# Optimization experiments

Hardware: AMD Instinct MI355X
Metric: run time of the kernel (lower is better)

## Reference

```python
import jax, jax.numpy as jnp
import numpy as np

N, B, D, K_IN, P = 64, 256, 1792, 35, 10
EPS = 1e-5


def setup_inputs() -> dict:
    key = jax.random.key(0)
    ks = jax.random.split(key, 8)
    s_tok = 1.0 / np.sqrt(K_IN)
    s_net = 1.0 / np.sqrt(D)
    return {
        "X": jax.random.normal(ks[0], (N, B, D), dtype=jnp.float32),
        "task_id": jax.random.normal(ks[1], (B, K_IN), dtype=jnp.float32),
        # tokens: Linear(35, 10*1792)
        "W_tok": jax.random.uniform(ks[2], (P * D, K_IN), jnp.float32, -s_tok, s_tok),
        "b_tok": jax.random.uniform(ks[3], (P * D,), jnp.float32, -s_tok, s_tok),
        # ptokens: Linear(35, 1792)
        "W_ptok": jax.random.uniform(ks[4], (D, K_IN), jnp.float32, -s_tok, s_tok),
        "b_ptok": jax.random.uniform(ks[5], (D,), jnp.float32, -s_tok, s_tok),
        # LayerNorm(1792)
        "gamma": jnp.ones((D,), jnp.float32),
        "beta": jnp.zeros((D,), jnp.float32),
        # net: Linear(1792, 10)
        "W_net": jax.random.uniform(ks[6], (P, D), jnp.float32, -s_net, s_net),
        "b_net": jax.random.uniform(ks[7], (P,), jnp.float32, -s_net, s_net),
    }


def _layernorm(x, gamma, beta):
    mu = jnp.mean(x, axis=-1, keepdims=True)
    var = jnp.mean(jnp.square(x - mu), axis=-1, keepdims=True)
    return (x - mu) * jax.lax.rsqrt(var + EPS) * gamma + beta


def reference(X, task_id, W_tok, b_tok, W_ptok, b_ptok, gamma, beta, W_net, b_net):
    # ptokens(task_id): (b, D); identical across n, so compute once and broadcast.
    ptok = task_id @ W_ptok.T + b_ptok                       # (b, D)
    task_token = _layernorm(ptok[None, :, :] + X, gamma, beta)  # (n, b, D)
    # net -> sigmoid: per-token mixing weights over P prompts.
    weight = jax.nn.sigmoid(task_token @ W_net.T + b_net)    # (n, b, P)
    # tokens(task_id): (b, P, D); identical across n, broadcast in einsum.
    prompt_bank = (task_id @ W_tok.T + b_tok).reshape(B, P, D)  # (b, P, D)
    prompt = jnp.einsum("nbp,bpd->nbd", weight, prompt_bank)  # (n, b, D)
    return X + prompt
```

## Files before the change

kernel.cpp:

```cpp
#include <hip/hip_runtime.h>
#include <hip/hip_bf16.h>

#define NN 64
#define BB 256
#define DD 1792
#define KK 35
#define PP 10
#define DQ 448
#define MROWS 16
#define NCHUNK 4
#define NGRP 28

__device__ __forceinline__ float group16_sum_dpp(float x) {
    asm("v_add_f32_dpp %0, %0, %0 row_shr:1 row_mask:0xf bank_mask:0xf bound_ctrl:0" : "+v"(x));
    asm("v_add_f32_dpp %0, %0, %0 row_shr:2 row_mask:0xf bank_mask:0xf bound_ctrl:0" : "+v"(x));
    asm("v_add_f32_dpp %0, %0, %0 row_shr:4 row_mask:0xf bank_mask:0xf bound_ctrl:0" : "+v"(x));
    asm("v_add_f32_dpp %0, %0, %0 row_shr:8 row_mask:0xf bank_mask:0xf bound_ctrl:0" : "+v"(x));
    return x;
}

__global__ void prep_gf(const float* __restrict__ gamma, const float* __restrict__ beta,
                        const float* __restrict__ Wnet, const float* __restrict__ bnet,
                        float* __restrict__ GF, float* __restrict__ SG, float* __restrict__ ZC) {
    const int p = blockIdx.x;
    const int tid = threadIdx.x;
    float sg = 0.f, sb = 0.f;
#pragma unroll
    for (int j = 0; j < 7; ++j) {
        int d = j * 256 + tid;
        float wv = Wnet[p * DD + d];
        float g = gamma[d] * wv;
        GF[p * DD + d] = g;
        sg += g;
        sb += beta[d] * wv;
    }
#pragma unroll
    for (int off = 32; off > 0; off >>= 1) {
        sg += __shfl_xor(sg, off);
        sb += __shfl_xor(sb, off);
    }
    __shared__ float rs[4][2];
    if ((tid & 63) == 0) { rs[tid >> 6][0] = sg; rs[tid >> 6][1] = sb; }
    __syncthreads();
    if (tid == 0) {
        float a = 0.f, c = 0.f;
#pragma unroll
        for (int w = 0; w < 4; ++w) { a += rs[w][0]; c += rs[w][1]; }
        SG[p] = a;
        ZC[p] = c + bnet[p];
    }
}

__global__ void prep_bank(const float* __restrict__ task,
                          const float* __restrict__ Wtok, const float* __restrict__ btok,
                          const float* __restrict__ Wptok, const float* __restrict__ bptok,
                          float* __restrict__ bank, float* __restrict__ ptok) {
    __shared__ float ti[32 * KK];
    const int tid = threadIdx.x;
    const int b0 = blockIdx.y * 32;
    for (int i = tid; i < 32 * KK; i += 256) ti[i] = task[b0 * KK + i];

    const int r = blockIdx.x * 256 + tid;
    const bool isbank = (r < PP * DD);
    const int rr = isbank ? r : (r - PP * DD);
    const float* __restrict__ W = isbank ? Wtok : Wptok;
    const float bias = isbank ? btok[r] : bptok[rr];

    float w[KK];
#pragma unroll
    for (int k = 0; k < KK; ++k) w[k] = W[rr * KK + k];

    __syncthreads();
#pragma unroll 1
    for (int bb = 0; bb < 32; ++bb) {
        float acc = bias;
#pragma unroll
        for (int k = 0; k < KK; ++k) acc = fmaf(ti[bb * KK + k], w[k], acc);
        const int b = b0 + bb;
        if (isbank) bank[b * (PP * DD) + r] = acc;
        else        ptok[b * DD + rr]       = acc;
    }
}

__global__ __launch_bounds__(448) void main_kernel(
    const float* __restrict__ X, const float* __restrict__ BANK,
    const float* __restrict__ PTOK, const float* __restrict__ GF,
    const float* __restrict__ SG, const float* __restrict__ ZC,
    float* __restrict__ OUT) {
    const int tid = threadIdx.x;
    const int b = blockIdx.y;
    const int n0 = blockIdx.x * MROWS;

    const float4* __restrict__ X4 = (const float4*)X;
    const float4* __restrict__ B4 = (const float4*)BANK;
    const float4* __restrict__ G4 = (const float4*)GF;
    const float4* __restrict__ P4 = (const float4*)PTOK;
    float4* __restrict__ O4 = (float4*)OUT;

    __shared__ float red[MROWS][NGRP][12];
    __shared__ float wlds[MROWS][PP];

    float4 gf[PP];
#pragma unroll
    for (int p = 0; p < PP; ++p) gf[p] = G4[p * DQ + tid];
    const float4 ptk = P4[b * DQ + tid];

    const bool writer = ((tid & 15) == 15);
    const int g = tid >> 4;

    float4 xn = X4[((n0 + 0) * BB + b) * DQ + tid];
#pragma unroll 1
    for (int r = 0; r < MROWS; ++r) {
        float4 x = xn;
        if (r < MROWS - 1) xn = X4[((n0 + r + 1) * BB + b) * DQ + tid];

        float4 t;
        t.x = x.x + ptk.x; t.y = x.y + ptk.y; t.z = x.z + ptk.z; t.w = x.w + ptk.w;

        float s1 = t.x + t.y + t.z + t.w;
        float s2 = t.x * t.x;
        s2 = fmaf(t.y, t.y, s2); s2 = fmaf(t.z, t.z, s2); s2 = fmaf(t.w, t.w, s2);
        float a[PP];
#pragma unroll
        for (int p = 0; p < PP; ++p) {
            float v = t.x * gf[p].x;
            v = fmaf(t.y, gf[p].y, v);
            v = fmaf(t.z, gf[p].z, v);
            v = fmaf(t.w, gf[p].w, v);
            a[p] = v;
        }
        s1 = group16_sum_dpp(s1);
        s2 = group16_sum_dpp(s2);
#pragma unroll
        for (int p = 0; p < PP; ++p) a[p] = group16_sum_dpp(a[p]);

        if (writer) {
            float4* dst = (float4*)&red[r][g][0];
            dst[0] = make_float4(s1, s2, a[0], a[1]);
            dst[1] = make_float4(a[2], a[3], a[4], a[5]);
            dst[2] = make_float4(a[6], a[7], a[8], a[9]);
        }
    }
    __syncthreads();

    if (tid < 256) {
        const int row = tid >> 4;
        const int v = tid & 15;
        float f = 0.f;
        if (v < 12) {
#pragma unroll
            for (int q = 0; q < NGRP; ++q) f += red[row][q][v];
        }
        const int base = (tid & 63) & ~15;
        const float mu = __shfl(f, base)     * (1.0f / (float)DD);
        const float ms = __shfl(f, base + 1) * (1.0f / (float)DD);
        const float istd = rsqrtf(ms - mu * mu + 1e-5f);
        if (v >= 2 && v < 12) {
            const int p = v - 2;
            const float z = istd * (f - mu * SG[p]) + ZC[p];
            wlds[row][p] = 1.0f / (1.0f + __expf(-z));
        }
    }
    __syncthreads();

    float4 bk[PP];
#pragma unroll
    for (int p = 0; p < PP; ++p) bk[p] = B4[(b * PP + p) * DQ + tid];

#pragma unroll 4
    for (int r = MROWS - 1; r >= 0; --r) {
        const int idx = ((n0 + r) * BB + b) * DQ + tid;
        float4 acc = X4[idx];
#pragma unroll
        for (int p = 0; p < PP; ++p) {
            const float wv2 = wlds[r][p];
            acc.x = fmaf(wv2, bk[p].x, acc.x);
            acc.y = fmaf(wv2, bk[p].y, acc.y);
            acc.z = fmaf(wv2, bk[p].z, acc.z);
            acc.w = fmaf(wv2, bk[p].w, acc.w);
        }
        O4[idx] = acc;
    }
}

extern "C" void kernel_launch(void* const* d_in, const int* in_sizes, int n_in,
                              void* d_out, int out_size, void* d_ws, size_t ws_size,
                              hipStream_t stream) {
    const float* X     = (const float*)d_in[0];
    const float* task  = (const float*)d_in[1];
    const float* Wtok  = (const float*)d_in[2];
    const float* btok  = (const float*)d_in[3];
    const float* Wptok = (const float*)d_in[4];
    const float* bptok = (const float*)d_in[5];
    const float* gamma = (const float*)d_in[6];
    const float* beta  = (const float*)d_in[7];
    const float* Wnet  = (const float*)d_in[8];
    const float* bnet  = (const float*)d_in[9];
    float* out = (float*)d_out;

    float* ws = (float*)d_ws;
    float* bank = ws;
    float* ptok = ws + (size_t)BB * PP * DD;
    float* GF   = ptok + (size_t)BB * DD;
    float* SG   = GF + PP * DD;
    float* ZC   = SG + PP;

    prep_gf<<<PP, 256, 0, stream>>>(gamma, beta, Wnet, bnet, GF, SG, ZC);
    prep_bank<<<dim3(77, 8), 256, 0, stream>>>(task, Wtok, btok, Wptok, bptok, bank, ptok);
    main_kernel<<<dim3(NCHUNK, BB), 448, 0, stream>>>(X, bank, ptok, GF, SG, ZC, out);
}
```

Baseline: 91.93 us.

## Keep X rows in registers across two half-passes to avoid rereading X

The main kernel now processes its 16 rows in two halves of 8. Each half loads its 8 X rows into registers once, computes the LayerNorm and net reductions from them, then reuses the same registers for the output mix. Before, X was read a second time from global memory in the output phase. This raises register pressure (8 float4 rows plus 10 bank/gf float4), may lower occupancy, adds an extra pair of barriers per half, and reloads GF and the bank slice twice per block.

```diff
diff --git a/kernel.cpp b/kernel.cpp
--- a/kernel.cpp
+++ b/kernel.cpp
@@ -8,6 +8,7 @@
 #define PP 10
 #define DQ 448
 #define MROWS 16
+#define HROWS 8
 #define NCHUNK 4
 #define NGRP 28
 
@@ -97,89 +98,93 @@
     const float4* __restrict__ P4 = (const float4*)PTOK;
     float4* __restrict__ O4 = (float4*)OUT;
 
-    __shared__ float red[MROWS][NGRP][12];
-    __shared__ float wlds[MROWS][PP];
-
-    float4 gf[PP];
-#pragma unroll
-    for (int p = 0; p < PP; ++p) gf[p] = G4[p * DQ + tid];
+    __shared__ float red[HROWS][NGRP][12];
+    __shared__ float wlds[HROWS][PP];
+
     const float4 ptk = P4[b * DQ + tid];
-
     const bool writer = ((tid & 15) == 15);
     const int g = tid >> 4;
 
-    float4 xn = X4[((n0 + 0) * BB + b) * DQ + tid];
 #pragma unroll 1
-    for (int r = 0; r < MROWS; ++r) {
-        float4 x = xn;
-        if (r < MROWS - 1) xn = X4[((n0 + r + 1) * BB + b) * DQ + tid];
-
-        float4 t;
-        t.x = x.x + ptk.x; t.y = x.y + ptk.y; t.z = x.z + ptk.z; t.w = x.w + ptk.w;
-
-        float s1 = t.x + t.y + t.z + t.w;
-        float s2 = t.x * t.x;
-        s2 = fmaf(t.y, t.y, s2); s2 = fmaf(t.z, t.z, s2); s2 = fmaf(t.w, t.w, s2);
-        float a[PP];
-#pragma unroll
-        for (int p = 0; p < PP; ++p) {
-            float v = t.x * gf[p].x;
-            v = fmaf(t.y, gf[p].y, v);
-            v = fmaf(t.z, gf[p].z, v);
-            v = fmaf(t.w, gf[p].w, v);
-            a[p] = v;
+    for (int half = 0; half < 2; ++half) {
+        const int r0 = n0 + half * HROWS;
+
+        float4 gf[PP];
+#pragma unroll
+        for (int p = 0; p < PP; ++p) gf[p] = G4[p * DQ + tid];
+        float4 x[HROWS];
+#pragma unroll
+        for (int r = 0; r < HROWS; ++r) x[r] = X4[((r0 + r) * BB + b) * DQ + tid];
+
+#pragma unroll
+        for (int r = 0; r < HROWS; ++r) {
+            float4 t;
+            t.x = x[r].x + ptk.x; t.y = x[r].y + ptk.y;
+            t.z = x[r].z + ptk.z; t.w = x[r].w + ptk.w;
+
+            float s1 = t.x + t.y + t.z + t.w;
+            float s2 = t.x * t.x;
+            s2 = fmaf(t.y, t.y, s2); s2 = fmaf(t.z, t.z, s2); s2 = fmaf(t.w, t.w, s2);
+            float a[PP];
+#pragma unroll
+            for (int p = 0; p < PP; ++p) {
+                float v = t.x * gf[p].x;
+                v = fmaf(t.y, gf[p].y, v);
+                v = fmaf(t.z, gf[p].z, v);
+                v = fmaf(t.w, gf[p].w, v);
+                a[p] = v;
+            }
+            s1 = group16_sum_dpp(s1);
+            s2 = group16_sum_dpp(s2);
+#pragma unroll
+            for (int p = 0; p < PP; ++p) a[p] = group16_sum_dpp(a[p]);
+
+            if (writer) {
+                float4* dst = (float4*)&red[r][g][0];
+                dst[0] = make_float4(s1, s2, a[0], a[1]);
+                dst[1] = make_float4(a[2], a[3], a[4], a[5]);
+                dst[2] = make_float4(a[6], a[7], a[8], a[9]);
+            }
         }
-        s1 = group16_sum_dpp(s1);
-        s2 = group16_sum_dpp(s2);
-#pragma unroll
-        for (int p = 0; p < PP; ++p) a[p] = group16_sum_dpp(a[p]);
-
-        if (writer) {
-            float4* dst = (float4*)&red[r][g][0];
-            dst[0] = make_float4(s1, s2, a[0], a[1]);
-            dst[1] = make_float4(a[2], a[3], a[4], a[5]);
-            dst[2] = make_float4(a[6], a[7], a[8], a[9]);
+        __syncthreads();
+
+        if (tid < HROWS * 16) {
+            const int row = tid >> 4;
+            const int v = tid & 15;
+            float f = 0.f;
+            if (v < 12) {
+#pragma unroll
+                for (int q = 0; q < NGRP; ++q) f += red[row][q][v];
+            }
+            const int base = (tid & 63) & ~15;
+            const float mu = __shfl(f, base)     * (1.0f / (float)DD);
+            const float ms = __shfl(f, base + 1) * (1.0f / (float)DD);
+            const float istd = rsqrtf(ms - mu * mu + 1e-5f);
+            if (v >= 2 && v < 12) {
+                const int p = v - 2;
+                const float z = istd * (f - mu * SG[p]) + ZC[p];
+                wlds[row][p] = 1.0f / (1.0f + __expf(-z));
+            }
         }
-    }
-    __syncthreads();
-
-    if (tid < 256) {
-        const int row = tid >> 4;
-        const int v = tid & 15;
-        float f = 0.f;
-        if (v < 12) {
-#pragma unroll
-            for (int q = 0; q < NGRP; ++q) f += red[row][q][v];
+        __syncthreads();
+
+        float4 bk[PP];
+#pragma unroll
+        for (int p = 0; p < PP; ++p) bk[p] = B4[(b * PP + p) * DQ + tid];
+
+#pragma unroll
+        for (int r = 0; r < HROWS; ++r) {
+            float4 acc = x[r];
+#pragma unroll
+            for (int p = 0; p < PP; ++p) {
+                const float wv = wlds[r][p];
+                acc.x = fmaf(wv, bk[p].x, acc.x);
+                acc.y = fmaf(wv, bk[p].y, acc.y);
+                acc.z = fmaf(wv, bk[p].z, acc.z);
+                acc.w = fmaf(wv, bk[p].w, acc.w);
+            }
+            O4[((r0 + r) * BB + b) * DQ + tid] = acc;
         }
-        const int base = (tid & 63) & ~15;
-        const float mu = __shfl(f, base)     * (1.0f / (float)DD);
-        const float ms = __shfl(f, base + 1) * (1.0f / (float)DD);
-        const float istd = rsqrtf(ms - mu * mu + 1e-5f);
-        if (v >= 2 && v < 12) {
-            const int p = v - 2;
-            const float z = istd * (f - mu * SG[p]) + ZC[p];
-            wlds[row][p] = 1.0f / (1.0f + __expf(-z));
-        }
-    }
-    __syncthreads();
-
-    float4 bk[PP];
-#pragma unroll
-    for (int p = 0; p < PP; ++p) bk[p] = B4[(b * PP + p) * DQ + tid];
-
-#pragma unroll 4
-    for (int r = MROWS - 1; r >= 0; --r) {
-        const int idx = ((n0 + r) * BB + b) * DQ + tid;
-        float4 acc = X4[idx];
-#pragma unroll
-        for (int p = 0; p < PP; ++p) {
-            const float wv2 = wlds[r][p];
-            acc.x = fmaf(wv2, bk[p].x, acc.x);
-            acc.y = fmaf(wv2, bk[p].y, acc.y);
-            acc.z = fmaf(wv2, bk[p].z, acc.z);
-            acc.w = fmaf(wv2, bk[p].w, acc.w);
-        }
-        O4[idx] = acc;
     }
 }
 
```

After: 95.08 us. 3.4% more time.
